# Kernel tuning notes

Measured on AMD Instinct MI355X. Metric: run time of the kernel, lower is better.

## Reference

```python
import jax, jax.numpy as jnp
import numpy as np

N_NODES = 50000
N_EDGES = 800000
IN_CH, HID_CH, OUT_CH = 128, 96, 40
NUM_LAYERS = 4
EPS = 1e-5          # torch BatchNorm1d default eps
ALPHA = 0.1         # GCNII residual coeff (missing arg in source; matches 0.9/0.1 blend)


def _xavier(key, fan_out, fan_in, gain=1.414):
    limit = gain * np.sqrt(6.0 / (fan_in + fan_out))
    return jax.random.uniform(key, (fan_out, fan_in), jnp.float32, -limit, limit)


def setup_inputs() -> dict:
    key = jax.random.key(0)
    ks = jax.random.split(key, 6)
    x = jax.random.normal(ks[0], (N_NODES, IN_CH), dtype=jnp.float32)
    edge_index = jax.random.randint(ks[1], (2, N_EDGES), 0, N_NODES, dtype=jnp.int64)
    W0 = _xavier(ks[2], HID_CH, IN_CH)
    W1 = _xavier(ks[3], HID_CH, HID_CH)
    W2 = _xavier(ks[4], HID_CH, HID_CH)
    W3 = _xavier(ks[5], OUT_CH, HID_CH)
    return {"x": x, "edge_index": edge_index, "W0": W0, "W1": W1, "W2": W2, "W3": W3}


def _norm_weights(src, dst, n):
    # remove existing self-loops, add one self-loop per node (weight handled separately)
    mask = (src != dst).astype(jnp.float32)
    deg = jax.ops.segment_sum(mask, dst, num_segments=n) + 1.0  # +1 for added self-loop
    dinv = jax.lax.rsqrt(deg)
    w = dinv[src] * dinv[dst] * mask           # [E] symmetric-normalized edge weights
    self_w = 1.0 / deg                          # self-loop weight deg^-0.5 * deg^-0.5
    return w, self_w


def _spmm(h, src, dst, w, self_w, n):
    # out[dst] = sum_e w_e * h[src_e]  +  self_w * h  (A^T @ h in the source)
    out = jax.ops.segment_sum(w[:, None] * h[src], dst, num_segments=n)
    return out + self_w[:, None] * h


def _bn(x):
    # BatchNorm1d(affine=False, track_running_stats=False): per-feature batch stats
    mu = x.mean(0)
    var = x.var(0)  # biased variance, as torch BN uses
    return (x - mu) * jax.lax.rsqrt(var + EPS)


def reference(x, edge_index, W0, W1, W2, W3):
    src, dst = edge_index[0], edge_index[1]
    n = x.shape[0]
    w, self_w = _norm_weights(src, dst, n)

    h = x @ W0.T
    h = jax.nn.relu(_bn(h))
    h0 = h  # x_ residual anchor; dropout is identity in eval mode

    for i, W in enumerate((W1, W2), start=1):  # i = 1 .. num_layers-2
        beta = 0.5 / i
        h = h * (1.0 - beta) + (h @ W.T) * beta
        h = (1.0 - ALPHA) * _spmm(h, src, dst, w, self_w, n) + ALPHA * h0  # conv_resi
        h = jax.nn.relu(_bn(h))

    h = h @ W3.T
    h = _spmm(h, src, dst, w, self_w, n)  # gcn_conv
    return h
```

## Files before the change

### kernel.cpp

```cpp
#include <hip/hip_runtime.h>

#define N_NODES 50000
#define N_EDGES 800000
#define IN_CH 128
#define HID_CH 96
#define OUT_CH 40
#define EPS 1e-5f
#define NREP 32

typedef __attribute__((ext_vector_type(8))) short bf16x8;
typedef __attribute__((ext_vector_type(4))) float f32x4;


__device__ __forceinline__ unsigned packbf(float a, float b) {
    unsigned ua = __float_as_uint(a), ub = __float_as_uint(b);
    ua += 0x7fffu + ((ua >> 16) & 1u);
    ub += 0x7fffu + ((ub >> 16) & 1u);
    return (ua >> 16) | (ub & 0xffff0000u);
}

struct f8 { float4 lo, hi; };

__device__ __forceinline__ f8 unpack8(uint4 v) {
    f8 r;
    r.lo = make_float4(__uint_as_float(v.x << 16), __uint_as_float(v.x & 0xffff0000u),
                       __uint_as_float(v.y << 16), __uint_as_float(v.y & 0xffff0000u));
    r.hi = make_float4(__uint_as_float(v.z << 16), __uint_as_float(v.z & 0xffff0000u),
                       __uint_as_float(v.w << 16), __uint_as_float(v.w & 0xffff0000u));
    return r;
}

__device__ __forceinline__ void up4(uint2 u, float* f) {
    f[0] = __uint_as_float(u.x << 16);
    f[1] = __uint_as_float(u.x & 0xffff0000u);
    f[2] = __uint_as_float(u.y << 16);
    f[3] = __uint_as_float(u.y & 0xffff0000u);
}


__global__ void count_kernel(const int* __restrict__ ei, int* __restrict__ cnt) {
    int e = blockIdx.x * blockDim.x + threadIdx.x;
    if (e >= N_EDGES) return;
    int s = ei[e], d = ei[N_EDGES + e];
    if (s != d) atomicAdd(&cnt[d], 1);
}

__global__ void norm_kernel(const int* __restrict__ cnt, float* __restrict__ dinv,
                            float* __restrict__ selfw) {
    int n = blockIdx.x * blockDim.x + threadIdx.x;
    if (n >= N_NODES) return;
    float deg = (float)(cnt[n] + 1);
    dinv[n]  = rsqrtf(deg);
    selfw[n] = 1.0f / deg;
}

__global__ void scan_kernel(const int* __restrict__ cnt, int* __restrict__ row_start) {
    __shared__ int partial[256];
    const int T = 256;
    int tid = threadIdx.x;
    int seg = (N_NODES + T - 1) / T;
    int s0 = tid * seg;
    int s1 = s0 + seg; if (s1 > N_NODES) s1 = N_NODES;
    int sum = 0;
    for (int i = s0; i < s1; i++) sum += cnt[i];
    partial[tid] = sum;
    __syncthreads();
    if (tid == 0) {
        int acc = 0;
        for (int i = 0; i < T; i++) { int v = partial[i]; partial[i] = acc; acc += v; }
    }
    __syncthreads();
    int acc = partial[tid];
    for (int i = s0; i < s1; i++) { row_start[i] = acc; acc += cnt[i]; }
    if (tid == T - 1) row_start[N_NODES] = acc;
}

__global__ void fill_kernel(const int* __restrict__ ei, const int* __restrict__ row_start,
                            int* __restrict__ fillp, const float* __restrict__ dinv,
                            int2* __restrict__ cw) {
    int e = blockIdx.x * blockDim.x + threadIdx.x;
    if (e >= N_EDGES) return;
    int s = ei[e], d = ei[N_EDGES + e];
    if (s == d) return;
    int p = atomicAdd(&fillp[d], 1);
    int idx = row_start[d] + p;
    cw[idx] = make_int2(s, __float_as_int(dinv[s] * dinv[d]));
}

__global__ void bn_fin(const float* __restrict__ stat, float* __restrict__ mu,
                       float* __restrict__ inv) {
    int c = threadIdx.x;
    if (c >= HID_CH) return;
    float s = 0.0f, q = 0.0f;
    for (int k = 0; k < NREP; k++) {
        s += stat[k * 2 * HID_CH + c];
        q += stat[k * 2 * HID_CH + HID_CH + c];
    }
    float m = s * (1.0f / N_NODES);
    float v = q * (1.0f / N_NODES) - m * m;
    mu[c] = m; inv[c] = rsqrtf(v + EPS);
}


template <int K, int C, int CG, bool XBF16, bool BLEND, bool NORMX, bool STATS, bool H0OUT>
__global__ __launch_bounds__(256, 4) void gemm7(
    const void* __restrict__ Xv, const float* __restrict__ W,
    unsigned* __restrict__ outb, unsigned* __restrict__ h0n,
    const float* __restrict__ muin, const float* __restrict__ invin,
    float* __restrict__ stat, float beta) {
    constexpr int K4 = K / 4;
    constexpr int KP2 = (K == 128) ? 68 : 52;
    constexpr int KS = K / 32;
    constexpr int CJ = CG / 16;
    __shared__ unsigned sW[CG * KP2];
    __shared__ unsigned sX[64 * KP2];
    __shared__ float sstat[STATS ? CG * 4 : 1];
    __shared__ float sstatq[STATS ? CG * 4 : 1];
    const int tid = threadIdx.x;
    const int lane = tid & 63;
    const int wid = tid >> 6;
    const int nbase = (int)blockIdx.x * 64;
    const float4* W4 = (const float4*)W;

    for (int i = tid; i < CG * K4; i += 256) {
        int o = i / K4, k4 = i - o * K4;
        uint2 pk = make_uint2(0u, 0u);
        if (o < C) {
            float4 wv = W4[(size_t)o * K4 + k4];
            pk.x = packbf(wv.x, wv.y); pk.y = packbf(wv.z, wv.w);
        }
        *(uint2*)&sW[o * KP2 + k4 * 2] = pk;
    }
    for (int i = tid; i < 64 * K4; i += 256) {
        int r = i / K4, k4 = i - r * K4;
        int n = nbase + r;
        float f[4] = {0.f, 0.f, 0.f, 0.f};
        if (n < N_NODES) {
            if (XBF16) {
                uint2 u = *(const uint2*)&((const unsigned*)Xv)[(size_t)n * (K / 2) + k4 * 2];
                up4(u, f);
            } else {
                float4 v = ((const float4*)Xv)[(size_t)n * K4 + k4];
                f[0] = v.x; f[1] = v.y; f[2] = v.z; f[3] = v.w;
            }
        }
        if (NORMX) {
            float4 m  = *(const float4*)&muin[k4 * 4];
            float4 iv = *(const float4*)&invin[k4 * 4];
            f[0] = fmaxf((f[0] - m.x) * iv.x, 0.0f);
            f[1] = fmaxf((f[1] - m.y) * iv.y, 0.0f);
            f[2] = fmaxf((f[2] - m.z) * iv.z, 0.0f);
            f[3] = fmaxf((f[3] - m.w) * iv.w, 0.0f);
        }
        uint2 pk; pk.x = packbf(f[0], f[1]); pk.y = packbf(f[2], f[3]);
        *(uint2*)&sX[r * KP2 + k4 * 2] = pk;
    }
    __syncthreads();

    const int r0 = wid * 16;
    const int l15 = lane & 15;
    const int koff = (lane >> 4) * 4;
    f32x4 acc[CJ];
#pragma unroll
    for (int j = 0; j < CJ; ++j) acc[j] = (f32x4){0.f, 0.f, 0.f, 0.f};

#pragma unroll
    for (int kk = 0; kk < KS; ++kk) {
        bf16x8 a = *(const bf16x8*)&sX[(r0 + l15) * KP2 + koff + kk * 16];
        bf16x8 b[CJ];
#pragma unroll
        for (int j = 0; j < CJ; ++j)
            b[j] = *(const bf16x8*)&sW[(j * 16 + l15) * KP2 + koff + kk * 16];
#pragma unroll
        for (int j = 0; j < CJ; ++j)
            acc[j] = __builtin_amdgcn_mfma_f32_16x16x32_bf16(a, b[j], acc[j], 0, 0, 0);
    }

    const int orow0 = r0 + ((lane >> 4) << 2);
#pragma unroll
    for (int j = 0; j < CJ; ++j) {
        const int c = j * 16 + l15;
#pragma unroll
        for (int q = 0; q < 4; ++q) {
            float v = acc[j][q];
            const int row = orow0 + q;
            if (BLEND) {
                unsigned u = sX[row * KP2 + (c >> 1)];
                float hv = __uint_as_float((c & 1) ? (u & 0xffff0000u) : (u << 16));
                v = (1.0f - beta) * hv + beta * v;
            }
            float p = __shfl_xor(v, 1);
            const int n = nbase + row;
            if (!(lane & 1) && n < N_NODES && c < C)
                outb[(size_t)n * (C / 2) + (c >> 1)] = packbf(v, p);
        }
        if (STATS) {
            float s = acc[j][0] + acc[j][1] + acc[j][2] + acc[j][3];
            float q2 = acc[j][0] * acc[j][0] + acc[j][1] * acc[j][1] +
                       acc[j][2] * acc[j][2] + acc[j][3] * acc[j][3];
            s  += __shfl_xor(s, 16);  s  += __shfl_xor(s, 32);
            q2 += __shfl_xor(q2, 16); q2 += __shfl_xor(q2, 32);
            if (lane < 16) {
                sstat[(j * 16 + lane) * 4 + wid] = s;
                sstatq[(j * 16 + lane) * 4 + wid] = q2;
            }
        }
    }

    if (H0OUT) {
        for (int i = tid; i < 64 * (C / 2); i += 256) {
            int r = i / (C / 2), c2 = i - r * (C / 2);
            int n = nbase + r;
            if (n < N_NODES) h0n[(size_t)n * (C / 2) + c2] = sX[r * KP2 + c2];
        }
    }

    if (STATS) {
        __syncthreads();
        if (tid < C) {
            float s = sstat[tid * 4] + sstat[tid * 4 + 1] + sstat[tid * 4 + 2] +
                      sstat[tid * 4 + 3];
            float q = sstatq[tid * 4] + sstatq[tid * 4 + 1] + sstatq[tid * 4 + 2] +
                      sstatq[tid * 4 + 3];
            const int rep = ((int)blockIdx.x & (NREP - 1)) * 2 * HID_CH;
            atomicAdd(&stat[rep + tid], s);
            atomicAdd(&stat[rep + HID_CH + tid], q);
        }
    }
}


template <int C, bool LAYER, bool STATS, bool PACKO>
__global__ __launch_bounds__(256) void spmm5(
    const uint4* __restrict__ tb, const uint4* __restrict__ h0n,
    const int* __restrict__ row_start, const int2* __restrict__ cw,
    const float* __restrict__ selfw, float* __restrict__ outf, uint4* __restrict__ outp,
    float* __restrict__ stat) {
    constexpr int C8 = C / 8;
    __shared__ float ssum[STATS ? C : 1];
    __shared__ float ssq[STATS ? C : 1];
    const int tid = threadIdx.x;
    if (STATS) {
        if (tid < C) { ssum[tid] = 0.0f; ssq[tid] = 0.0f; }
        __syncthreads();
    }
    const int total = N_NODES * C8;
    for (int idx = blockIdx.x * 256 + tid; idx < total; idx += gridDim.x * 256) {
        const int n = idx / C8;
        const int c8 = idx - n * C8;
        const float sw = selfw[n];
        f8 acc = unpack8(tb[idx]);
        acc.lo.x *= sw; acc.lo.y *= sw; acc.lo.z *= sw; acc.lo.w *= sw;
        acc.hi.x *= sw; acc.hi.y *= sw; acc.hi.z *= sw; acc.hi.w *= sw;
        const int rs = row_start[n], re = row_start[n + 1];
        int j = rs;
        for (; j + 3 < re; j += 4) {
            int2 e0 = cw[j], e1 = cw[j + 1], e2 = cw[j + 2], e3 = cw[j + 3];
            uint4 p0 = tb[(size_t)e0.x * C8 + c8];
            uint4 p1 = tb[(size_t)e1.x * C8 + c8];
            uint4 p2 = tb[(size_t)e2.x * C8 + c8];
            uint4 p3 = tb[(size_t)e3.x * C8 + c8];
            float w0 = __int_as_float(e0.y), w1 = __int_as_float(e1.y);
            float w2 = __int_as_float(e2.y), w3 = __int_as_float(e3.y);
            f8 a0 = unpack8(p0), a1 = unpack8(p1), a2 = unpack8(p2), a3 = unpack8(p3);
            acc.lo.x = fmaf(w0, a0.lo.x, acc.lo.x); acc.lo.y = fmaf(w0, a0.lo.y, acc.lo.y);
            acc.lo.z = fmaf(w0, a0.lo.z, acc.lo.z); acc.lo.w = fmaf(w0, a0.lo.w, acc.lo.w);
            acc.hi.x = fmaf(w0, a0.hi.x, acc.hi.x); acc.hi.y = fmaf(w0, a0.hi.y, acc.hi.y);
            acc.hi.z = fmaf(w0, a0.hi.z, acc.hi.z); acc.hi.w = fmaf(w0, a0.hi.w, acc.hi.w);
            acc.lo.x = fmaf(w1, a1.lo.x, acc.lo.x); acc.lo.y = fmaf(w1, a1.lo.y, acc.lo.y);
            acc.lo.z = fmaf(w1, a1.lo.z, acc.lo.z); acc.lo.w = fmaf(w1, a1.lo.w, acc.lo.w);
            acc.hi.x = fmaf(w1, a1.hi.x, acc.hi.x); acc.hi.y = fmaf(w1, a1.hi.y, acc.hi.y);
            acc.hi.z = fmaf(w1, a1.hi.z, acc.hi.z); acc.hi.w = fmaf(w1, a1.hi.w, acc.hi.w);
            acc.lo.x = fmaf(w2, a2.lo.x, acc.lo.x); acc.lo.y = fmaf(w2, a2.lo.y, acc.lo.y);
            acc.lo.z = fmaf(w2, a2.lo.z, acc.lo.z); acc.lo.w = fmaf(w2, a2.lo.w, acc.lo.w);
            acc.hi.x = fmaf(w2, a2.hi.x, acc.hi.x); acc.hi.y = fmaf(w2, a2.hi.y, acc.hi.y);
            acc.hi.z = fmaf(w2, a2.hi.z, acc.hi.z); acc.hi.w = fmaf(w2, a2.hi.w, acc.hi.w);
            acc.lo.x = fmaf(w3, a3.lo.x, acc.lo.x); acc.lo.y = fmaf(w3, a3.lo.y, acc.lo.y);
            acc.lo.z = fmaf(w3, a3.lo.z, acc.lo.z); acc.lo.w = fmaf(w3, a3.lo.w, acc.lo.w);
            acc.hi.x = fmaf(w3, a3.hi.x, acc.hi.x); acc.hi.y = fmaf(w3, a3.hi.y, acc.hi.y);
            acc.hi.z = fmaf(w3, a3.hi.z, acc.hi.z); acc.hi.w = fmaf(w3, a3.hi.w, acc.hi.w);
        }
        for (; j < re; ++j) {
            int2 e0 = cw[j];
            uint4 p0 = tb[(size_t)e0.x * C8 + c8];
            float w0 = __int_as_float(e0.y);
            f8 a0 = unpack8(p0);
            acc.lo.x = fmaf(w0, a0.lo.x, acc.lo.x); acc.lo.y = fmaf(w0, a0.lo.y, acc.lo.y);
            acc.lo.z = fmaf(w0, a0.lo.z, acc.lo.z); acc.lo.w = fmaf(w0, a0.lo.w, acc.lo.w);
            acc.hi.x = fmaf(w0, a0.hi.x, acc.hi.x); acc.hi.y = fmaf(w0, a0.hi.y, acc.hi.y);
            acc.hi.z = fmaf(w0, a0.hi.z, acc.hi.z); acc.hi.w = fmaf(w0, a0.hi.w, acc.hi.w);
        }
        if (LAYER) {
            f8 h0 = unpack8(h0n[idx]);
            acc.lo.x = 0.9f * acc.lo.x + 0.1f * h0.lo.x;
            acc.lo.y = 0.9f * acc.lo.y + 0.1f * h0.lo.y;
            acc.lo.z = 0.9f * acc.lo.z + 0.1f * h0.lo.z;
            acc.lo.w = 0.9f * acc.lo.w + 0.1f * h0.lo.w;
            acc.hi.x = 0.9f * acc.hi.x + 0.1f * h0.hi.x;
            acc.hi.y = 0.9f * acc.hi.y + 0.1f * h0.hi.y;
            acc.hi.z = 0.9f * acc.hi.z + 0.1f * h0.hi.z;
            acc.hi.w = 0.9f * acc.hi.w + 0.1f * h0.hi.w;
        }
        if (PACKO) {
            uint4 pk;
            pk.x = packbf(acc.lo.x, acc.lo.y); pk.y = packbf(acc.lo.z, acc.lo.w);
            pk.z = packbf(acc.hi.x, acc.hi.y); pk.w = packbf(acc.hi.z, acc.hi.w);
            outp[idx] = pk;
        } else {
            float* op = outf + (size_t)n * C + c8 * 8;
            *(float4*)op = acc.lo;
            *(float4*)(op + 4) = acc.hi;
        }
        if (STATS) {
            int c = c8 * 8;
            atomicAdd(&ssum[c + 0], acc.lo.x); atomicAdd(&ssq[c + 0], acc.lo.x * acc.lo.x);
            atomicAdd(&ssum[c + 1], acc.lo.y); atomicAdd(&ssq[c + 1], acc.lo.y * acc.lo.y);
            atomicAdd(&ssum[c + 2], acc.lo.z); atomicAdd(&ssq[c + 2], acc.lo.z * acc.lo.z);
            atomicAdd(&ssum[c + 3], acc.lo.w); atomicAdd(&ssq[c + 3], acc.lo.w * acc.lo.w);
            atomicAdd(&ssum[c + 4], acc.hi.x); atomicAdd(&ssq[c + 4], acc.hi.x * acc.hi.x);
            atomicAdd(&ssum[c + 5], acc.hi.y); atomicAdd(&ssq[c + 5], acc.hi.y * acc.hi.y);
            atomicAdd(&ssum[c + 6], acc.hi.z); atomicAdd(&ssq[c + 6], acc.hi.z * acc.hi.z);
            atomicAdd(&ssum[c + 7], acc.hi.w); atomicAdd(&ssq[c + 7], acc.hi.w * acc.hi.w);
        }
    }
    if (STATS) {
        __syncthreads();
        if (tid < C) {
            const int rep = ((int)blockIdx.x & (NREP - 1)) * 2 * HID_CH;
            atomicAdd(&stat[rep + tid], ssum[tid]);
            atomicAdd(&stat[rep + HID_CH + tid], ssq[tid]);
        }
    }
}


extern "C" void kernel_launch(void* const* d_in, const int* in_sizes, int n_in,
                              void* d_out, int out_size, void* d_ws, size_t ws_size,
                              hipStream_t stream) {
    const float* x  = (const float*)d_in[0];
    const int*   ei = (const int*)d_in[1];
    const float* W0 = (const float*)d_in[2];
    const float* W1 = (const float*)d_in[3];
    const float* W2 = (const float*)d_in[4];
    const float* W3 = (const float*)d_in[5];
    float* out = (float*)d_out;

    char* w = (char*)d_ws;
    auto alloc = [&](size_t bytes) {
        void* p = (void*)w;
        w += (bytes + 255) & ~(size_t)255;
        return p;
    };
    const int STATB = NREP * 2 * HID_CH;
    int*      cnt       = (int*)alloc(N_NODES * 4);
    int*      row_start = (int*)alloc((N_NODES + 1) * 4);
    int*      fillp     = (int*)alloc(N_NODES * 4);
    int2*     cw        = (int2*)alloc((size_t)N_EDGES * 8);
    float*    dinv      = (float*)alloc(N_NODES * 4);
    float*    selfw     = (float*)alloc(N_NODES * 4);
    unsigned* g0b       = (unsigned*)alloc((size_t)N_NODES * (HID_CH / 2) * 4);
    unsigned* sb        = (unsigned*)alloc((size_t)N_NODES * (HID_CH / 2) * 4);
    unsigned* tb        = (unsigned*)alloc((size_t)N_NODES * (HID_CH / 2) * 4);
    unsigned* h0n       = (unsigned*)alloc((size_t)N_NODES * (HID_CH / 2) * 4);
    float*    stat0     = (float*)alloc(STATB * 4);
    float*    stat1     = (float*)alloc(STATB * 4);
    float*    stat2     = (float*)alloc(STATB * 4);
    float*    mu0  = (float*)alloc(HID_CH * 4);
    float*    inv0 = (float*)alloc(HID_CH * 4);
    float*    mu1  = (float*)alloc(HID_CH * 4);
    float*    inv1 = (float*)alloc(HID_CH * 4);
    float*    mu2  = (float*)alloc(HID_CH * 4);
    float*    inv2 = (float*)alloc(HID_CH * 4);

    const int EB = (N_EDGES + 255) / 256;
    const int NB = (N_NODES + 255) / 256;
    const int G64 = (N_NODES + 63) / 64;

    hipMemsetAsync(cnt, 0, N_NODES * 4, stream);
    hipMemsetAsync(fillp, 0, N_NODES * 4, stream);
    hipMemsetAsync(stat0, 0, (size_t)STATB * 3 * 4 + 512, stream);

    count_kernel<<<EB, 256, 0, stream>>>(ei, cnt);
    norm_kernel<<<NB, 256, 0, stream>>>(cnt, dinv, selfw);
    scan_kernel<<<1, 256, 0, stream>>>(cnt, row_start);
    fill_kernel<<<EB, 256, 0, stream>>>(ei, row_start, fillp, dinv, cw);

    gemm7<IN_CH, HID_CH, 96, false, false, false, true, false>
        <<<G64, 256, 0, stream>>>(x, W0, g0b, nullptr, nullptr, nullptr, stat0, 0.0f);
    bn_fin<<<1, HID_CH, 0, stream>>>(stat0, mu0, inv0);

    gemm7<HID_CH, HID_CH, 96, true, true, true, false, true>
        <<<G64, 256, 0, stream>>>(g0b, W1, tb, h0n, mu0, inv0, nullptr, 0.5f);
    spmm5<HID_CH, true, true, true><<<2344, 256, 0, stream>>>(
        (const uint4*)tb, (const uint4*)h0n, row_start, cw, selfw, nullptr, (uint4*)sb, stat1);
    bn_fin<<<1, HID_CH, 0, stream>>>(stat1, mu1, inv1);

    gemm7<HID_CH, HID_CH, 96, true, true, true, false, false>
        <<<G64, 256, 0, stream>>>(sb, W2, tb, nullptr, mu1, inv1, nullptr, 0.25f);
    spmm5<HID_CH, true, true, true><<<2344, 256, 0, stream>>>(
        (const uint4*)tb, (const uint4*)h0n, row_start, cw, selfw, nullptr, (uint4*)sb, stat2);
    bn_fin<<<1, HID_CH, 0, stream>>>(stat2, mu2, inv2);

    gemm7<HID_CH, OUT_CH, 48, true, false, true, false, false>
        <<<G64, 256, 0, stream>>>(sb, W3, tb, nullptr, mu2, inv2, nullptr, 0.0f);
    spmm5<OUT_CH, false, false, false><<<977, 256, 0, stream>>>(
        (const uint4*)tb, nullptr, row_start, cw, selfw, out, nullptr, nullptr);
}
```

Measured before the change: 477.8 us.

## Replace single-block serial CSR scan with three-pass parallel block scan

Replaces the single-block serial prefix sum over node degree counts with a three-kernel parallel scan: per-block reductions, a scan of the block sums, then a per-block wavefront scan. The final pass also computes the normalization factors and zeroes the fill counters. This removes the separate norm kernel and one memset. The aim is to remove the serialized scan bottleneck at the cost of an extra small launch.

Result: faster. 394.1 us (-17.5%).

```diff
diff --git a/kernel.cpp b/kernel.cpp
--- a/kernel.cpp
+++ b/kernel.cpp
@@ -7,6 +7,7 @@
 #define OUT_CH 40
 #define EPS 1e-5f
 #define NREP 32
+#define NBK 196
 
 typedef __attribute__((ext_vector_type(8))) short bf16x8;
 typedef __attribute__((ext_vector_type(4))) float f32x4;
@@ -45,34 +46,65 @@
     if (s != d) atomicAdd(&cnt[d], 1);
 }
 
-__global__ void norm_kernel(const int* __restrict__ cnt, float* __restrict__ dinv,
-                            float* __restrict__ selfw) {
-    int n = blockIdx.x * blockDim.x + threadIdx.x;
-    if (n >= N_NODES) return;
-    float deg = (float)(cnt[n] + 1);
-    dinv[n]  = rsqrtf(deg);
-    selfw[n] = 1.0f / deg;
-}
-
-__global__ void scan_kernel(const int* __restrict__ cnt, int* __restrict__ row_start) {
-    __shared__ int partial[256];
-    const int T = 256;
-    int tid = threadIdx.x;
-    int seg = (N_NODES + T - 1) / T;
-    int s0 = tid * seg;
-    int s1 = s0 + seg; if (s1 > N_NODES) s1 = N_NODES;
-    int sum = 0;
-    for (int i = s0; i < s1; i++) sum += cnt[i];
-    partial[tid] = sum;
+__global__ void scan_a(const int* __restrict__ cnt, int* __restrict__ bsum) {
+    int i = blockIdx.x * 256 + threadIdx.x;
+    int v = (i < N_NODES) ? cnt[i] : 0;
+#pragma unroll
+    for (int d = 1; d < 64; d <<= 1) v += __shfl_xor(v, d);
+    __shared__ int ws[4];
+    if ((threadIdx.x & 63) == 0) ws[threadIdx.x >> 6] = v;
     __syncthreads();
-    if (tid == 0) {
-        int acc = 0;
-        for (int i = 0; i < T; i++) { int v = partial[i]; partial[i] = acc; acc += v; }
-    }
+    if (threadIdx.x == 0) bsum[blockIdx.x] = ws[0] + ws[1] + ws[2] + ws[3];
+}
+
+__global__ void scan_b(const int* __restrict__ bsum, int* __restrict__ bexc,
+                       int* __restrict__ row_start) {
+    const int tid = threadIdx.x;
+    const int lane = tid & 63;
+    const int wid = tid >> 6;
+    int v = (tid < NBK) ? bsum[tid] : 0;
+    int inc = v;
+#pragma unroll
+    for (int d = 1; d < 64; d <<= 1) {
+        int t = __shfl_up(inc, d);
+        if (lane >= d) inc += t;
+    }
+    __shared__ int ws[4];
+    if (lane == 63) ws[wid] = inc;
     __syncthreads();
-    int acc = partial[tid];
-    for (int i = s0; i < s1; i++) { row_start[i] = acc; acc += cnt[i]; }
-    if (tid == T - 1) row_start[N_NODES] = acc;
+    int woff = 0;
+    for (int k = 0; k < 4; k++) if (k < wid) woff += ws[k];
+    int exc = inc - v + woff;
+    if (tid < NBK) bexc[tid] = exc;
+    if (tid == NBK - 1) row_start[N_NODES] = exc + v;
+}
+
+__global__ void scan_c(const int* __restrict__ cnt, const int* __restrict__ bexc,
+                       int* __restrict__ row_start, float* __restrict__ dinv,
+                       float* __restrict__ selfw, int* __restrict__ fillp) {
+    const int tid = threadIdx.x;
+    const int lane = tid & 63;
+    const int wid = tid >> 6;
+    const int i = blockIdx.x * 256 + tid;
+    int v = (i < N_NODES) ? cnt[i] : 0;
+    int inc = v;
+#pragma unroll
+    for (int d = 1; d < 64; d <<= 1) {
+        int t = __shfl_up(inc, d);
+        if (lane >= d) inc += t;
+    }
+    __shared__ int ws[4];
+    if (lane == 63) ws[wid] = inc;
+    __syncthreads();
+    int woff = 0;
+    for (int k = 0; k < 4; k++) if (k < wid) woff += ws[k];
+    if (i < N_NODES) {
+        row_start[i] = bexc[blockIdx.x] + woff + inc - v;
+        float deg = (float)(v + 1);
+        dinv[i]  = rsqrtf(deg);
+        selfw[i] = 1.0f / deg;
+        fillp[i] = 0;
+    }
 }
 
 __global__ void fill_kernel(const int* __restrict__ ei, const int* __restrict__ row_start,
@@ -355,6 +387,8 @@
     int*      cnt       = (int*)alloc(N_NODES * 4);
     int*      row_start = (int*)alloc((N_NODES + 1) * 4);
     int*      fillp     = (int*)alloc(N_NODES * 4);
+    int*      bsum      = (int*)alloc(NBK * 4);
+    int*      bexc      = (int*)alloc(NBK * 4);
     int2*     cw        = (int2*)alloc((size_t)N_EDGES * 8);
     float*    dinv      = (float*)alloc(N_NODES * 4);
     float*    selfw     = (float*)alloc(N_NODES * 4);
@@ -373,16 +407,15 @@
     float*    inv2 = (float*)alloc(HID_CH * 4);
 
     const int EB = (N_EDGES + 255) / 256;
-    const int NB = (N_NODES + 255) / 256;
     const int G64 = (N_NODES + 63) / 64;
 
     hipMemsetAsync(cnt, 0, N_NODES * 4, stream);
-    hipMemsetAsync(fillp, 0, N_NODES * 4, stream);
     hipMemsetAsync(stat0, 0, (size_t)STATB * 3 * 4 + 512, stream);
 
     count_kernel<<<EB, 256, 0, stream>>>(ei, cnt);
-    norm_kernel<<<NB, 256, 0, stream>>>(cnt, dinv, selfw);
-    scan_kernel<<<1, 256, 0, stream>>>(cnt, row_start);
+    scan_a<<<NBK, 256, 0, stream>>>(cnt, bsum);
+    scan_b<<<1, 256, 0, stream>>>(bsum, bexc, row_start);
+    scan_c<<<NBK, 256, 0, stream>>>(cnt, bexc, row_start, dinv, selfw, fillp);
     fill_kernel<<<EB, 256, 0, stream>>>(ei, row_start, fillp, dinv, cw);
 
     gemm7<IN_CH, HID_CH, 96, false, false, false, true, false>
```
